# Kernel optimization log

Hardware: AMD Instinct MI355X
Metric: run time of the kernel (lower is better)

Reference implementation:

```python
import jax, jax.numpy as jnp
import numpy as np

NUM_GRAPHS = 1024
NODES_PER_GRAPH = 9
EDGES_PER_GRAPH = NODES_PER_GRAPH * (NODES_PER_GRAPH - 1)  # 72, fully connected no self-loops
N = NUM_GRAPHS * NODES_PER_GRAPH
E = NUM_GRAPHS * EDGES_PER_GRAPH
POS_DIM = 64
HID = 256          # gnn_hidden_dim / common_gnn_dim
S1_FEAT = HID      # stage1 feature_dim (after projection)
S1_INT = S1_FEAT + POS_DIM           # 320
S2_FEAT = 2 * HID                    # 512 (two scales concatenated)
S2_OUT = 2 * HID                     # 512
S2_INT = S2_FEAT + POS_DIM           # 576
LN_EPS = 1e-5
SM_EPS = 1e-16  # PyG softmax eps


def _dense(x, w, b):
    return x @ w + b


def _layer_norm(x, g, b):
    mu = jnp.mean(x, axis=-1, keepdims=True)
    var = jnp.mean(jnp.square(x - mu), axis=-1, keepdims=True)
    return (x - mu) * jax.lax.rsqrt(var + LN_EPS) * g + b


def _segment_softmax(logits, idx, n):
    # logits: [E,1]; normalize over edges sharing the same destination node
    m = jax.ops.segment_max(logits, idx, num_segments=n)
    e = jnp.exp(logits - m[idx])
    s = jax.ops.segment_sum(e, idx, num_segments=n)
    return e / (s[idx] + SM_EPS)


def _gnn_layer(x, pos, src, dst, n, p):
    # x: [N, F], pos: [N, P]; edges src->dst (PyG: edge_index[0]=src j, edge_index[1]=dst i)
    ix = jnp.concatenate([x, pos], axis=-1)            # integrated_x [N, F+P]
    ii, ij = ix[dst], ix[src]                          # integrated_x_i / _j per edge
    # pairwise_fn(integrated_x_j, integrated_x_i) -> mlp(cat([integrated_x_i, integrated_x_j]))
    pw_in = jnp.concatenate([ii, ij], axis=-1)         # [E, 2*(F+P)]
    rel = _dense(jax.nn.gelu(_dense(pw_in, p['pw1_w'], p['pw1_b']), approximate=False),
                 p['pw2_w'], p['pw2_b'])               # [E, out]
    att_in = jnp.concatenate([x[dst], x[src], pos[dst], pos[src]], axis=-1)
    logits = _dense(jax.nn.leaky_relu(_dense(att_in, p['att1_w'], p['att1_b']), 0.01),
                    p['att2_w'], p['att2_b'])          # [E, 1]
    attw = _segment_softmax(logits, dst, n)
    aggr = jax.ops.segment_sum(attw * rel, dst, num_segments=n)  # [N, out]
    upd = jax.nn.gelu(_dense(jnp.concatenate([ix, aggr], axis=-1), p['upd_w'], p['upd_b']),
                      approximate=False)
    h = _dense(ix, p['skip_w'], p['skip_b']) + upd
    return _layer_norm(h, p['ln_g'], p['ln_b'])


def _glorot(key, shape):
    fan_in, fan_out = shape[0], shape[1]
    lim = np.sqrt(6.0 / (fan_in + fan_out))
    return jax.random.uniform(key, shape, jnp.float32, -lim, lim)


def setup_inputs() -> dict:
    key = jax.random.key(0)
    ks = iter(jax.random.split(key, 64))

    feat_low = jax.random.normal(next(ks), (N, 512), jnp.float32)
    feat_high = jax.random.normal(next(ks), (N, 1024), jnp.float32)
    batch_indices = jnp.repeat(jnp.arange(NUM_GRAPHS), NODES_PER_GRAPH).astype(jnp.int32)

    # fully connected (no self loop) edges within each 9-node graph
    loc = np.array([(j, i) for i in range(NODES_PER_GRAPH) for j in range(NODES_PER_GRAPH) if i != j],
                   dtype=np.int64)  # (src, dst)
    off = np.repeat(np.arange(NUM_GRAPHS) * NODES_PER_GRAPH, EDGES_PER_GRAPH)
    src = np.tile(loc[:, 0], NUM_GRAPHS) + off
    dst = np.tile(loc[:, 1], NUM_GRAPHS) + off
    edge_index = jnp.asarray(np.stack([src, dst]), dtype=jnp.int32)  # [2, E]

    inp = dict(feat_low=feat_low, feat_high=feat_high,
               batch_indices=batch_indices, edge_index=edge_index)

    inp['pos_table'] = jax.random.normal(next(ks), (NODES_PER_GRAPH, POS_DIM), jnp.float32)
    inp['proj_low_w'] = _glorot(next(ks), (512, HID)); inp['proj_low_b'] = jnp.zeros((HID,), jnp.float32)
    inp['proj_high_w'] = _glorot(next(ks), (1024, HID)); inp['proj_high_b'] = jnp.zeros((HID,), jnp.float32)

    def layer_params(pref, fdim, pdim, out):
        integ = fdim + pdim
        d = {}
        d[pref + 'pw1_w'] = _glorot(next(ks), (2 * integ, out)); d[pref + 'pw1_b'] = jnp.zeros((out,), jnp.float32)
        d[pref + 'pw2_w'] = _glorot(next(ks), (out, out)); d[pref + 'pw2_b'] = jnp.zeros((out,), jnp.float32)
        d[pref + 'att1_w'] = _glorot(next(ks), (2 * fdim + 2 * pdim, out)); d[pref + 'att1_b'] = jnp.zeros((out,), jnp.float32)
        d[pref + 'att2_w'] = _glorot(next(ks), (out, 1)); d[pref + 'att2_b'] = jnp.zeros((1,), jnp.float32)
        d[pref + 'upd_w'] = _glorot(next(ks), (integ + out, out)); d[pref + 'upd_b'] = jnp.zeros((out,), jnp.float32)
        d[pref + 'ln_g'] = jnp.ones((out,), jnp.float32); d[pref + 'ln_b'] = jnp.zeros((out,), jnp.float32)
        d[pref + 'skip_w'] = _glorot(next(ks), (integ, out)); d[pref + 'skip_b'] = jnp.zeros((out,), jnp.float32)
        return d

    inp.update(layer_params('s1_', S1_FEAT, POS_DIM, HID))
    inp.update(layer_params('s2_', S2_FEAT, POS_DIM, S2_OUT))

    inp['cls1_w'] = _glorot(next(ks), (S2_OUT, HID)); inp['cls1_b'] = jnp.zeros((HID,), jnp.float32)
    inp['cls2_w'] = _glorot(next(ks), (HID, 1)); inp['cls2_b'] = jnp.zeros((1,), jnp.float32)
    return inp


def _forward(feat_low, feat_high, pos_table,
             proj_low_w, proj_low_b, proj_high_w, proj_high_b,
             s1, s2, cls1_w, cls1_b, cls2_w, cls2_b,
             batch_indices, edge_index):
    src, dst = edge_index[0], edge_index[1]
    pos_ids = jnp.tile(jnp.arange(NODES_PER_GRAPH), NUM_GRAPHS)
    pos = pos_table[pos_ids]                                  # [N, P]
    h_low = _gnn_layer(_dense(feat_low, proj_low_w, proj_low_b), pos, src, dst, N, s1)
    h_high = _gnn_layer(_dense(feat_high, proj_high_w, proj_high_b), pos, src, dst, N, s1)
    unified = jnp.concatenate([h_low, h_high], axis=-1)       # [N, 512]
    h2 = _gnn_layer(unified, pos, src, dst, N, s2)            # [N, 512]
    pooled = jax.ops.segment_sum(h2, batch_indices, num_segments=NUM_GRAPHS)
    hid = jax.nn.gelu(_dense(pooled, cls1_w, cls1_b), approximate=False)
    return _dense(hid, cls2_w, cls2_b)                        # [G, 1]


S1_KEYS = ['pw1_w', 'pw1_b', 'pw2_w', 'pw2_b', 'att1_w', 'att1_b', 'att2_w', 'att2_b',
           'upd_w', 'upd_b', 'ln_g', 'ln_b', 'skip_w', 'skip_b']


def reference(feat_low, feat_high, batch_indices, edge_index, pos_table,
              proj_low_w, proj_low_b, proj_high_w, proj_high_b,
              s1_pw1_w, s1_pw1_b, s1_pw2_w, s1_pw2_b, s1_att1_w, s1_att1_b,
              s1_att2_w, s1_att2_b, s1_upd_w, s1_upd_b, s1_ln_g, s1_ln_b,
              s1_skip_w, s1_skip_b,
              s2_pw1_w, s2_pw1_b, s2_pw2_w, s2_pw2_b, s2_att1_w, s2_att1_b,
              s2_att2_w, s2_att2_b, s2_upd_w, s2_upd_b, s2_ln_g, s2_ln_b,
              s2_skip_w, s2_skip_b,
              cls1_w, cls1_b, cls2_w, cls2_b):
    s1 = dict(zip(S1_KEYS, [s1_pw1_w, s1_pw1_b, s1_pw2_w, s1_pw2_b, s1_att1_w, s1_att1_b,
                            s1_att2_w, s1_att2_b, s1_upd_w, s1_upd_b, s1_ln_g, s1_ln_b,
                            s1_skip_w, s1_skip_b]))
    s2 = dict(zip(S1_KEYS, [s2_pw1_w, s2_pw1_b, s2_pw2_w, s2_pw2_b, s2_att1_w, s2_att1_b,
                            s2_att2_w, s2_att2_b, s2_upd_w, s2_upd_b, s2_ln_g, s2_ln_b,
                            s2_skip_w, s2_skip_b]))
    return _forward(feat_low, feat_high, pos_table,
                    proj_low_w, proj_low_b, proj_high_w, proj_high_b,
                    s1, s2, cls1_w, cls1_b, cls2_w, cls2_b,
                    batch_indices, edge_index)
```

## Files before the change

### kernel.cpp

```cpp
#include <hip/hip_runtime.h>
#include <math.h>

#define NUM_GRAPHS 1024
#define NPG 9
#define NN 9216
#define NN2 18432
#define POSD 64

typedef __attribute__((ext_vector_type(8))) short bf16x8;
typedef __attribute__((ext_vector_type(4))) float f32x4;

__device__ __forceinline__ float gelu_f(float x) {
    return 0.5f * x * (1.0f + erff(x * 0.70710678118654752f));
}
__device__ __forceinline__ float gelu_fast(float x) {
    float y = 0.7978845608f * x * (1.0f + 0.044715f * x * x);
    float t = __expf(-2.0f * fabsf(y));
    float r = (1.0f - t) / (1.0f + t);
    r = copysignf(r, y);
    return 0.5f * x * (1.0f + r);
}
__device__ __forceinline__ ushort f2b(float v) {
    unsigned u = __float_as_uint(v);
    return (ushort)((u + 0x7fffu + ((u >> 16) & 1u)) >> 16);
}
__device__ __forceinline__ float b2f(ushort u) {
    return __uint_as_float(((unsigned)u) << 16);
}
__device__ __forceinline__ void gload16(const ushort* g, ushort* l) {
    __builtin_amdgcn_global_load_lds((const __attribute__((address_space(1))) void*)g,
                                     (__attribute__((address_space(3))) void*)l, 16, 0, 0);
}

__global__ __launch_bounds__(256, 3) void mgemm(
    const ushort* __restrict__ A, int lda,
    const ushort* __restrict__ Wt, int ldw,
    const float* __restrict__ bias1,
    const float* __restrict__ prow, int ldp,
    float* outF, ushort* outB, int ldo,
    long partStride, int K)
{
    __shared__ ushort sA[3][128 * 32];
    __shared__ ushort sB[3][128 * 32];
    const int wv = threadIdx.x >> 6, lane = threadIdx.x & 63;
    const int rh = wv & 1, ch = wv >> 1;

    const int GX = gridDim.x;
    const int nwg = GX * gridDim.y;
    const int flat = blockIdx.y * GX + blockIdx.x;
    const int swq = nwg >> 3, swr = nwg & 7;
    const int xcd = flat & 7, posi = flat >> 3;
    const int tix = (xcd < swr ? xcd * (swq + 1) : swr * (swq + 1) + (xcd - swr) * swq) + posi;
    const int m0 = (tix / GX) * 128, n0 = (tix % GX) * 128;

    const int koff = blockIdx.z * K;

    f32x4 acc[4][4];
#pragma unroll
    for (int i = 0; i < 4; i++)
#pragma unroll
        for (int j = 0; j < 4; j++) acc[i][j] = (f32x4){0.f, 0.f, 0.f, 0.f};

    const ushort* Ab = A + (size_t)m0 * lda + koff;
    const ushort* Wb = Wt + (size_t)n0 * ldw + koff;
    if (outF) outF += (size_t)blockIdx.z * partStride;

    auto stage = [&](int b, int k0) {
#pragma unroll
        for (int i = 0; i < 2; i++) {
            int c = wv * 2 + i;
            int u = c * 64 + lane;
            int row = u >> 2, p = u & 3;
            int q = (p - (row >> 1)) & 3;
            gload16(Ab + (size_t)row * lda + k0 + q * 8, sA[b] + c * 512);
            gload16(Wb + (size_t)row * ldw + k0 + q * 8, sB[b] + c * 512);
        }
    };

    const int nsteps = K >> 5;
    stage(0, 0);
    stage(1, 32);
    int cur = 0;
    for (int s = 0; s < nsteps; s++) {
        if (s + 1 < nsteps) {
            asm volatile("s_waitcnt vmcnt(4)" ::: "memory");
        } else {
            asm volatile("s_waitcnt vmcnt(0)" ::: "memory");
        }
        __builtin_amdgcn_s_barrier();
        __builtin_amdgcn_sched_barrier(0);
        if (s + 2 < nsteps) {
            int nb = cur + 2; if (nb >= 3) nb -= 3;
            stage(nb, (s + 2) << 5);
        }

        const int qg = lane >> 4;
        bf16x8 af[4], bfr[4];
#pragma unroll
        for (int bi = 0; bi < 4; bi++) {
            int r = rh * 64 + bi * 16 + (lane & 15);
            af[bi] = *(const bf16x8*)(sA[cur] + (r * 4 + ((qg + (r >> 1)) & 3)) * 8);
        }
#pragma unroll
        for (int bj = 0; bj < 4; bj++) {
            int r = ch * 64 + bj * 16 + (lane & 15);
            bfr[bj] = *(const bf16x8*)(sB[cur] + (r * 4 + ((qg + (r >> 1)) & 3)) * 8);
        }
        __builtin_amdgcn_s_setprio(1);
#pragma unroll
        for (int bi = 0; bi < 4; bi++)
#pragma unroll
            for (int bj = 0; bj < 4; bj++)
                acc[bi][bj] = __builtin_amdgcn_mfma_f32_16x16x32_bf16(
                    af[bi], bfr[bj], acc[bi][bj], 0, 0, 0);
        __builtin_amdgcn_s_setprio(0);
        __builtin_amdgcn_sched_barrier(0);
        cur++; if (cur >= 3) cur -= 3;
    }

    float* sP = (float*)sA;
    const bool haveP = (prow != 0);
    if (haveP) {
        __syncthreads();
        for (int i = threadIdx.x; i < 9 * 128; i += 256) {
            int rr = i >> 7, c = i & 127;
            sP[rr * 129 + c] = prow[(size_t)rr * ldp + n0 + c] + bias1[n0 + c];
        }
        __syncthreads();
    }

#pragma unroll
    for (int bi = 0; bi < 4; bi++) {
#pragma unroll
        for (int r = 0; r < 4; r++) {
            int m = m0 + rh * 64 + bi * 16 + (lane >> 4) * 4 + r;
            int r9 = m % 9;
#pragma unroll
            for (int bj = 0; bj < 4; bj++) {
                int nc = ch * 64 + bj * 16 + (lane & 15);
                int n = n0 + nc;
                float v = acc[bi][bj][r];
                if (haveP) v += sP[r9 * 129 + nc];
                if (outF) outF[(size_t)m * ldo + n] = v;
                if (outB) outB[(size_t)m * ldo + n] = f2b(v);
            }
        }
    }
}

#define NJOBS 16
struct TJobsArg {
    const float* src[NJOBS];
    long dst[NJOBS];
    int K[NJOBS], N[NJOBS], off0[NJOBS], ldo[NJOBS];
};

__global__ __launch_bounds__(256) void tw_kernel(TJobsArg ja, ushort* wbuf)
{
    int j = blockIdx.y;
    int K = ja.K[j], N = ja.N[j];
    int tk = K >> 5, tn = N >> 5;
    int t = blockIdx.x;
    if (t >= tk * tn) return;
    int kt = t % tk, nt = t / tk;
    const float* src = ja.src[j];
    ushort* out = wbuf + ja.dst[j];
    int ldo = ja.ldo[j];
    __shared__ float L[32][33];
    int r = threadIdx.x >> 5, c = threadIdx.x & 31;
#pragma unroll
    for (int rr = 0; rr < 4; rr++) {
        int k = kt * 32 + rr * 8 + r;
        L[rr * 8 + r][c] = src[(size_t)(ja.off0[j] + k) * N + nt * 32 + c];
    }
    __syncthreads();
#pragma unroll
    for (int rr = 0; rr < 4; rr++) {
        int n = nt * 32 + rr * 8 + r;
        out[(size_t)n * ldo + kt * 32 + c] = f2b(L[c][rr * 8 + r]);
    }
}

__global__ void pjred_kernel(const float* __restrict__ PT,
                             const float* __restrict__ bl, const float* __restrict__ bh,
                             ushort* __restrict__ ixa1)
{
    int i = blockIdx.x * 256 + threadIdx.x;
    if (i >= NN2 * 64) return;
    int n = i >> 6, cq = i & 63;
    const float *p0, *p1, *bb; int r;
    if (n < NN) { p0 = PT; p1 = PT + (size_t)NN * 256; bb = bl; r = n; }
    else { p0 = PT + (size_t)2 * NN * 256; p1 = PT + (size_t)3 * NN * 256; bb = bh; r = n - NN; }
    float4 a = ((const float4*)(p0 + (size_t)r * 256))[cq];
    float4 b = ((const float4*)(p1 + (size_t)r * 256))[cq];
    float4 bs = ((const float4*)bb)[cq];
    ushort4 o;
    o.x = f2b(a.x + b.x + bs.x); o.y = f2b(a.y + b.y + bs.y);
    o.z = f2b(a.z + b.z + bs.z); o.w = f2b(a.w + b.w + bs.w);
    ((ushort4*)(ixa1 + (size_t)n * 512))[cq] = o;
}

__global__ __launch_bounds__(256) void edge_kernel(
    const ushort* __restrict__ PB, const float* __restrict__ att2_w,
    ushort* __restrict__ Gout, int ldG, float* __restrict__ S, int O, int cshift)
{
    __shared__ ushort sPB[9 * 2048];
    __shared__ float sAw[512];
    __shared__ float logits[72];
    __shared__ float aw[72];
    const int g = blockIdx.x;
    const int tid = threadIdx.x, lane = tid & 63, wave = tid >> 6;
    const int O4 = O * 4, O5 = O * 5;
    const int cpr = O >> 7;
    const int total = 9 * cpr;
    const ushort* gbase = PB + (size_t)g * 9 * O5;

    for (int i = wave; i < total; i += 4) {
        int row = i / cpr, co = i - row * cpr;
        gload16(gbase + (size_t)row * O5 + co * 512 + lane * 8, sPB + i * 512);
    }
    for (int c = tid; c < O; c += 256) sAw[c] = att2_w[c];
    __syncthreads();

    for (int e = wave; e < 72; e += 4) {
        int d = e >> 3, k = e & 7;
        int s = k + (k >= d);
        const ushort* ad = sPB + d * O4 + 2 * O;
        const ushort* as = sPB + s * O4 + 3 * O;
        float p = 0.f;
        for (int c0 = lane * 4; c0 < O; c0 += 256) {
            ushort4 a4 = *(const ushort4*)(ad + c0);
            ushort4 s4 = *(const ushort4*)(as + c0);
            const ushort* ap = (const ushort*)&a4;
            const ushort* sp = (const ushort*)&s4;
#pragma unroll
            for (int j = 0; j < 4; j++) {
                float v = b2f(ap[j]) + b2f(sp[j]);
                v = v > 0.f ? v : 0.01f * v;
                p += v * sAw[c0 + j];
            }
        }
#pragma unroll
        for (int off = 32; off; off >>= 1) p += __shfl_down(p, off, 64);
        if (lane == 0) logits[e] = p;
    }
    __syncthreads();

    if (tid < 9) {
        float m = -INFINITY;
#pragma unroll
        for (int k = 0; k < 8; k++) m = fmaxf(m, logits[tid * 8 + k]);
        float s = 0.f, ee[8];
#pragma unroll
        for (int k = 0; k < 8; k++) { ee[k] = expf(logits[tid * 8 + k] - m); s += ee[k]; }
        float inv = 1.0f / (s + 1e-16f);
#pragma unroll
        for (int k = 0; k < 8; k++) aw[tid * 8 + k] = ee[k] * inv;
        S[g * 9 + tid] = s * inv;
    }
    __syncthreads();

    const int nch = O >> 3;
    for (int idx = tid; idx < 9 * nch; idx += 256) {
        int n = idx >> cshift, cc = idx & (nch - 1);
        bf16x8 pdv = *(const bf16x8*)(sPB + n * O4 + cc * 8);
        const ushort* pp = (const ushort*)&pdv;
        float acc8[8];
#pragma unroll
        for (int j = 0; j < 8; j++) acc8[j] = 0.f;
#pragma unroll
        for (int k = 0; k < 8; k++) {
            int s = k + (k >= n);
            float w = aw[n * 8 + k];
            bf16x8 psv = *(const bf16x8*)(sPB + s * O4 + O + cc * 8);
            const ushort* qp = (const ushort*)&psv;
#pragma unroll
            for (int j = 0; j < 8; j++)
                acc8[j] += w * gelu_fast(b2f(pp[j]) + b2f(qp[j]));
        }
        ushort o8[8];
#pragma unroll
        for (int j = 0; j < 8; j++) o8[j] = f2b(acc8[j]);
        *(bf16x8*)(Gout + (size_t)(g * 9 + n) * ldG + cc * 8) = *(const bf16x8*)o8;
    }
}

__global__ __launch_bounds__(256) void ln_kernel(
    const float* __restrict__ P0, const float* __restrict__ P1,
    const float* __restrict__ ub, const float* __restrict__ vb,
    const float* __restrict__ S, const float* __restrict__ posU,
    const ushort* __restrict__ PBs, int ld5,
    const float* __restrict__ gw, const float* __restrict__ bw,
    ushort* outB, int ldoB, int rowsplit, float* outF, int O)
{
    __shared__ float sm[4];
    const int n = blockIdx.x, tid = threadIdx.x;
    const int lane = tid & 63, wid = tid >> 6;
    const float* p0 = P0 + (size_t)n * O;
    const float* p1 = P1 + (size_t)n * O;
    const ushort* sr = PBs + (size_t)n * ld5;
    const float* pu = posU + (size_t)(n % 9) * O;
    const float sv = S[n];
    const int cnt = O >> 8;

    float vals[2];
    float sum = 0.f;
#pragma unroll
    for (int i = 0; i < 2; i++) {
        if (i < cnt) {
            int c = tid + 256 * i;
            float t = p0[c] + p1[c] + ub[c] + vb[c] * sv + pu[c];
            vals[i] = gelu_f(t) + b2f(sr[c]);
            sum += vals[i];
        }
    }
#pragma unroll
    for (int off = 32; off; off >>= 1) sum += __shfl_down(sum, off, 64);
    if (lane == 0) sm[wid] = sum;
    __syncthreads();
    const float mu = (sm[0] + sm[1] + sm[2] + sm[3]) / (float)O;
    __syncthreads();

    float var = 0.f;
#pragma unroll
    for (int i = 0; i < 2; i++) {
        if (i < cnt) { float d = vals[i] - mu; var += d * d; }
    }
#pragma unroll
    for (int off = 32; off; off >>= 1) var += __shfl_down(var, off, 64);
    if (lane == 0) sm[wid] = var;
    __syncthreads();
    const float rstd = rsqrtf((sm[0] + sm[1] + sm[2] + sm[3]) / (float)O + 1e-5f);

    int orow = n, coloff = 0;
    if (n >= rowsplit) { orow = n - rowsplit; coloff = 256; }
#pragma unroll
    for (int i = 0; i < 2; i++) {
        if (i < cnt) {
            int c = tid + 256 * i;
            float v = (vals[i] - mu) * rstd * gw[c] + bw[c];
            if (outB) outB[(size_t)orow * ldoB + coloff + c] = f2b(v);
            if (outF) outF[(size_t)n * O + c] = v;
        }
    }
}

__global__ void prep_kernel(
    const float* __restrict__ pw1_b1, const float* __restrict__ att1_b1, const float* __restrict__ skip_b1,
    const float* __restrict__ pw1_b2, const float* __restrict__ att1_b2, const float* __restrict__ skip_b2,
    const float* __restrict__ pos_table,
    const float* __restrict__ s1_pw1, const float* __restrict__ s1_att, const float* __restrict__ s1_skp,
    const float* __restrict__ s2_pw1, const float* __restrict__ s2_att, const float* __restrict__ s2_skp,
    const float* __restrict__ pw2_b1, const float* __restrict__ upd_w1,
    const float* __restrict__ pw2_b2, const float* __restrict__ upd_w2,
    const float* __restrict__ pw2_w1, const float* __restrict__ pw2_w2,
    const float* __restrict__ feat_low, const float* __restrict__ feat_high,
    float* biasC1, float* biasC2,
    float* posPB1, float* posPB2, float* posU1, float* posU2,
    float* vb1, float* vb2, ushort* pw2f1, ushort* pw2f2, ushort* featB)
{
    int i = blockIdx.x * 256 + threadIdx.x;
    if (i < 1280) {
        float v;
        if (i < 256) v = pw1_b1[i];
        else if (i < 512) v = 0.f;
        else if (i < 768) v = att1_b1[i - 512];
        else if (i < 1024) v = 0.f;
        else v = skip_b1[i - 1024];
        biasC1[i] = v;
        return;
    }
    i -= 1280;
    if (i < 2560) {
        float v;
        if (i < 512) v = pw1_b2[i];
        else if (i < 1024) v = 0.f;
        else if (i < 1536) v = att1_b2[i - 1024];
        else if (i < 2048) v = 0.f;
        else v = skip_b2[i - 2048];
        biasC2[i] = v;
        return;
    }
    i -= 2560;
    if (i < 9 * 1280) {
        int r = i / 1280, n = i - r * 1280;
        int sec = n >> 8, c = n & 255;
        const float* src; int row0;
        if (sec == 0) { src = s1_pw1; row0 = 256; }
        else if (sec == 1) { src = s1_pw1; row0 = 576; }
        else if (sec == 2) { src = s1_att; row0 = 512; }
        else if (sec == 3) { src = s1_att; row0 = 576; }
        else { src = s1_skp; row0 = 256; }
        float a = 0.f;
        for (int k = 0; k < 64; k++) a += pos_table[r * 64 + k] * src[(size_t)(row0 + k) * 256 + c];
        posPB1[i] = a;
        return;
    }
    i -= 9 * 1280;
    if (i < 9 * 2560) {
        int r = i / 2560, n = i - r * 2560;
        int sec = n >> 9, c = n & 511;
        const float* src; int row0;
        if (sec == 0) { src = s2_pw1; row0 = 512; }
        else if (sec == 1) { src = s2_pw1; row0 = 1088; }
        else if (sec == 2) { src = s2_att; row0 = 1024; }
        else if (sec == 3) { src = s2_att; row0 = 1088; }
        else { src = s2_skp; row0 = 512; }
        float a = 0.f;
        for (int k = 0; k < 64; k++) a += pos_table[r * 64 + k] * src[(size_t)(row0 + k) * 512 + c];
        posPB2[i] = a;
        return;
    }
    i -= 9 * 2560;
    if (i < 9 * 256) {
        int r = i >> 8, c = i & 255;
        float a = 0.f;
        for (int k = 0; k < 64; k++) a += pos_table[r * 64 + k] * upd_w1[(size_t)(256 + k) * 256 + c];
        posU1[i] = a;
        return;
    }
    i -= 9 * 256;
    if (i < 9 * 512) {
        int r = i >> 9, c = i & 511;
        float a = 0.f;
        for (int k = 0; k < 64; k++) a += pos_table[r * 64 + k] * upd_w2[(size_t)(512 + k) * 512 + c];
        posU2[i] = a;
        return;
    }
    i -= 9 * 512;
    if (i < 256) {
        float a = 0.f;
        for (int j = 0; j < 256; j++) a += pw2_b1[j] * upd_w1[(size_t)(320 + j) * 256 + i];
        vb1[i] = a;
        return;
    }
    i -= 256;
    if (i < 512) {
        float a = 0.f;
        for (int j = 0; j < 512; j++) a += pw2_b2[j] * upd_w2[(size_t)(576 + j) * 512 + i];
        vb2[i] = a;
        return;
    }
    i -= 512;
    if (i < 256 * 256) { pw2f1[i] = f2b(pw2_w1[i]); return; }
    i -= 256 * 256;
    if (i < 512 * 512) { pw2f2[i] = f2b(pw2_w2[i]); return; }
    i -= 512 * 512;
    if (i < NN * 512 / 4) {
        float4 v = ((const float4*)feat_low)[i];
        ushort4 o;
        o.x = f2b(v.x); o.y = f2b(v.y); o.z = f2b(v.z); o.w = f2b(v.w);
        ((ushort4*)featB)[i] = o;
        return;
    }
    i -= NN * 512 / 4;
    if (i < NN * 1024 / 4) {
        float4 v = ((const float4*)feat_high)[i];
        ushort4 o;
        o.x = f2b(v.x); o.y = f2b(v.y); o.z = f2b(v.z); o.w = f2b(v.w);
        ((ushort4*)(featB + (size_t)NN * 512))[i] = o;
    }
}

__global__ __launch_bounds__(256) void head_kernel(
    const float* __restrict__ h2,
    const float* __restrict__ cls1_w, const float* __restrict__ cls1_b,
    const float* __restrict__ cls2_w, const float* __restrict__ cls2_b,
    float* __restrict__ out)
{
    __shared__ float pooled[4][512];
    __shared__ float hid[4][256];
    const int b = blockIdx.x, tid = threadIdx.x;

    for (int idx = tid; idx < 4 * 512; idx += 256) {
        int gi = idx >> 9, c = idx & 511;
        const float* base = h2 + (size_t)((b * 4 + gi) * 9) * 512 + c;
        float s = 0.f;
#pragma unroll
        for (int k = 0; k < NPG; k++) s += base[(size_t)k * 512];
        pooled[gi][c] = s;
    }
    __syncthreads();

    {
        float acc[4] = {0.f, 0.f, 0.f, 0.f};
        for (int c = 0; c < 512; c++) {
            float w = cls1_w[(size_t)c * 256 + tid];
#pragma unroll
            for (int gi = 0; gi < 4; gi++) acc[gi] += pooled[gi][c] * w;
        }
        float bb = cls1_b[tid];
#pragma unroll
        for (int gi = 0; gi < 4; gi++) hid[gi][tid] = gelu_f(acc[gi] + bb);
    }
    __syncthreads();

    {
        int gi = tid >> 6, lane = tid & 63;
        float p = 0.f;
#pragma unroll
        for (int i = 0; i < 4; i++) p += hid[gi][lane + 64 * i] * cls2_w[lane + 64 * i];
#pragma unroll
        for (int off = 32; off; off >>= 1) p += __shfl_down(p, off, 64);
        if (lane == 0) out[b * 4 + gi] = p + cls2_b[0];
    }
}

static inline void mg(hipStream_t st, int M, int N, int K,
                      const ushort* A, int lda, const ushort* Wt, int ldw,
                      const float* bias1, const float* prow, int ldp,
                      float* outF, ushort* outB, int ldo,
                      int nz, long partStride)
{
    dim3 grid(N / 128, M / 128, nz);
    mgemm<<<grid, dim3(256), 0, st>>>(A, lda, Wt, ldw, bias1, prow, ldp,
                                      outF, outB, ldo, partStride, K);
}

extern "C" void kernel_launch(void* const* d_in, const int* in_sizes, int n_in,
                              void* d_out, int out_size, void* d_ws, size_t ws_size,
                              hipStream_t stream)
{
    (void)in_sizes; (void)n_in; (void)out_size; (void)ws_size;
    const float* feat_low   = (const float*)d_in[0];
    const float* feat_high  = (const float*)d_in[1];
    const float* pos_table  = (const float*)d_in[4];
    const float* proj_low_w  = (const float*)d_in[5];
    const float* proj_low_b  = (const float*)d_in[6];
    const float* proj_high_w = (const float*)d_in[7];
    const float* proj_high_b = (const float*)d_in[8];
    const float* cls1_w = (const float*)d_in[37];
    const float* cls1_b = (const float*)d_in[38];
    const float* cls2_w = (const float*)d_in[39];
    const float* cls2_b = (const float*)d_in[40];
    float* out = (float*)d_out;

    const float* s1_pw1 = (const float*)d_in[9];
    const float* s1_att = (const float*)d_in[13];
    const float* s1_upd = (const float*)d_in[17];
    const float* s1_skp = (const float*)d_in[21];
    const float* s2_pw1 = (const float*)d_in[23];
    const float* s2_att = (const float*)d_in[27];
    const float* s2_upd = (const float*)d_in[31];
    const float* s2_skp = (const float*)d_in[35];

    const float* att2_w1 = (const float*)d_in[15];
    const float* upd_b1  = (const float*)d_in[18];
    const float* ln_g1   = (const float*)d_in[19];
    const float* ln_b1   = (const float*)d_in[20];
    const float* att2_w2 = (const float*)d_in[29];
    const float* upd_b2  = (const float*)d_in[32];
    const float* ln_g2   = (const float*)d_in[33];
    const float* ln_b2   = (const float*)d_in[34];

    char* base = (char*)d_ws;
    size_t cur = 0;
    auto alloc = [&](size_t bytes) { void* p = base + cur; cur += (bytes + 255) & ~(size_t)255; return p; };
    void*   PBreg = alloc((size_t)NN * 2560 * 2);
    ushort* PB    = (ushort*)PBreg;
    ushort* featB = (ushort*)PBreg;
    void*   IX1reg = alloc((size_t)NN2 * 512 * 2);
    ushort* ixa1  = (ushort*)IX1reg;
    float*  h2    = (float*)IX1reg;
    ushort* ixa2  = (ushort*)alloc((size_t)NN * 1024 * 2);
    float*  PT    = (float*)alloc((size_t)4 * NN * 256 * 4);
    float*  S     = (float*)alloc((size_t)NN2 * 4);
    float*  biasC1 = (float*)alloc(1280 * 4);
    float*  biasC2 = (float*)alloc(2560 * 4);
    float*  posPB1 = (float*)alloc(9 * 1280 * 4);
    float*  posPB2 = (float*)alloc(9 * 2560 * 4);
    float*  posU1  = (float*)alloc(9 * 256 * 4);
    float*  posU2  = (float*)alloc(9 * 512 * 4);
    float*  vb1   = (float*)alloc(256 * 4);
    float*  vb2   = (float*)alloc(512 * 4);
    ushort* wbuf  = (ushort*)alloc((size_t)3400000 * 2);

    TJobsArg ja;
    long woff[16];
    {
        struct J { const float* s; int K, N, off0, ldo; long sz; };
        J js[NJOBS] = {
            {proj_low_w,  512, 256, 0, 512, 512L * 256},
            {proj_high_w, 1024, 256, 0, 1024, 1024L * 256},
            {s1_pw1, 256, 256, 0, 256, 256L * 256},
            {s1_pw1, 256, 256, 320, 256, 256L * 256},
            {s1_att, 256, 256, 0, 256, 256L * 256},
            {s1_att, 256, 256, 256, 256, 256L * 256},
            {s1_skp, 256, 256, 0, 256, 256L * 256},
            {s1_upd, 256, 256, 0, 512, 512L * 256},
            {s1_upd, 256, 256, 320, 256, 256L * 256},
            {s2_pw1, 512, 512, 0, 512, 512L * 512},
            {s2_pw1, 512, 512, 576, 512, 512L * 512},
            {s2_att, 512, 512, 0, 512, 512L * 512},
            {s2_att, 512, 512, 512, 512, 512L * 512},
            {s2_skp, 512, 512, 0, 512, 512L * 512},
            {s2_upd, 512, 512, 0, 1024, 1024L * 512},
            {s2_upd, 512, 512, 576, 512, 512L * 512},
        };
        long off = 0;
        for (int i = 0; i < NJOBS; i++) {
            ja.src[i] = js[i].s; ja.K[i] = js[i].K; ja.N[i] = js[i].N;
            ja.off0[i] = js[i].off0; ja.ldo[i] = js[i].ldo;
            ja.dst[i] = off; woff[i] = off;
            off += js[i].sz;
        }
    }
    long pw2off1 = woff[15] + 512L * 512;
    long pw2off2 = pw2off1 + 256L * 256;
    tw_kernel<<<dim3(256, NJOBS), dim3(256), 0, stream>>>(ja, wbuf);

    ushort* wBig5_1 = wbuf + woff[2];
    ushort* updW1   = wbuf + woff[7];
    ushort* updbT1  = wbuf + woff[8];
    ushort* wBig5_2 = wbuf + woff[9];
    ushort* updW2   = wbuf + woff[14];
    ushort* updbT2  = wbuf + woff[15];
    ushort* pw2f1   = wbuf + pw2off1;
    ushort* pw2f2   = wbuf + pw2off2;

    {
        long tot = 1280 + 2560 + 9 * 1280 + 9 * 2560 + 9 * 256 + 9 * 512
                 + 256 + 512 + 256 * 256 + 512 * 512
                 + (long)NN * 512 / 4 + (long)NN * 1024 / 4;
        prep_kernel<<<dim3((unsigned)((tot + 255) / 256)), dim3(256), 0, stream>>>(
            (const float*)d_in[10], (const float*)d_in[14], (const float*)d_in[22],
            (const float*)d_in[24], (const float*)d_in[28], (const float*)d_in[36],
            pos_table,
            s1_pw1, s1_att, s1_skp, s2_pw1, s2_att, s2_skp,
            (const float*)d_in[12], s1_upd, (const float*)d_in[26], s2_upd,
            (const float*)d_in[11], (const float*)d_in[25],
            feat_low, feat_high,
            biasC1, biasC2, posPB1, posPB2, posU1, posU2, vb1, vb2, pw2f1, pw2f2, featB);
    }

    mg(stream, 256, 256, 256, updbT1, 256, pw2f1, 256, 0, 0, 0, 0, updW1 + 256, 512, 1, 0);
    mg(stream, 512, 512, 512, updbT2, 512, pw2f2, 512, 0, 0, 0, 0, updW2 + 512, 1024, 1, 0);

    mg(stream, NN, 256, 256, featB, 512, wbuf + woff[0], 512, 0, 0, 0,
       PT, 0, 256, 2, (long)NN * 256);
    mg(stream, NN, 256, 512, featB + (size_t)NN * 512, 1024, wbuf + woff[1], 1024, 0, 0, 0,
       PT + (size_t)2 * NN * 256, 0, 256, 2, (long)NN * 256);
    pjred_kernel<<<dim3(NN2 * 64 / 256), dim3(256), 0, stream>>>(PT, proj_low_b, proj_high_b, ixa1);

    mg(stream, NN2, 1280, 256, ixa1, 512, wBig5_1, 256, biasC1, posPB1, 1280, 0, PB, 1280, 1, 0);
    edge_kernel<<<dim3(2 * NUM_GRAPHS), dim3(256), 0, stream>>>(
        PB, att2_w1, ixa1 + 256, 512, S, 256, 5);
    mg(stream, NN2, 256, 256, ixa1, 512, updW1, 512, 0, 0, 0, PT, 0, 256, 2, (long)NN2 * 256);
    ln_kernel<<<dim3(NN2), dim3(256), 0, stream>>>(
        PT, PT + (size_t)NN2 * 256, upd_b1, vb1, S, posU1,
        PB + 4 * 256, 1280, ln_g1, ln_b1, ixa2, 1024, NN, 0, 256);

    mg(stream, NN, 2560, 512, ixa2, 1024, wBig5_2, 512, biasC2, posPB2, 2560, 0, PB, 2560, 1, 0);
    edge_kernel<<<dim3(NUM_GRAPHS), dim3(256), 0, stream>>>(
        PB, att2_w2, ixa2 + 512, 1024, S, 512, 6);
    mg(stream, NN, 512, 512, ixa2, 1024, updW2, 1024, 0, 0, 0, PT, 0, 512, 2, (long)NN * 512);
    ln_kernel<<<dim3(NN), dim3(256), 0, stream>>>(
        PT, PT + (size_t)NN * 512, upd_b2, vb2, S, posU2,
        PB + 4 * 512, 2560, ln_g2, ln_b2, 0, 0, 1 << 30, h2, 512);

    head_kernel<<<dim3(NUM_GRAPHS / 4), dim3(256), 0, stream>>>(h2, cls1_w, cls1_b, cls2_w, cls2_b, out);
}
```

Before: 552.2 us.

## Fuse projection GEMMs with bias/bf16 epilogue and drop split-K for update GEMMs

Replaces the two split-K projection GEMMs and the separate reduction kernel with one batched pjgemm kernel. It uses a triple-buffered LDS pipeline with swizzled loads and XCD-aware tile remapping, and writes bias-added bf16 directly into the stage-1 input buffer. The update GEMMs now run with a full K and a single split, so ln_kernel reads one partial buffer instead of summing two. This removes the fp32 partial-sum round trips and a kernel launch, but the update GEMMs have fewer workgroups and so less parallelism.

```diff
diff --git a/kernel.cpp b/kernel.cpp
--- a/kernel.cpp
+++ b/kernel.cpp
@@ -143,6 +143,118 @@
                 if (haveP) v += sP[r9 * 129 + nc];
                 if (outF) outF[(size_t)m * ldo + n] = v;
                 if (outB) outB[(size_t)m * ldo + n] = f2b(v);
+            }
+        }
+    }
+}
+
+struct PJArg {
+    const ushort* A[2];
+    const ushort* W[2];
+    const float*  bias[2];
+    ushort*       out[2];
+    int lda[2], K[2];
+};
+
+__global__ __launch_bounds__(256, 3) void pjgemm(PJArg pa)
+{
+    __shared__ ushort sA[3][128 * 32];
+    __shared__ ushort sB[3][128 * 32];
+    const int z = blockIdx.z;
+    const ushort* __restrict__ A  = pa.A[z];
+    const ushort* __restrict__ Wt = pa.W[z];
+    const float*  __restrict__ bias = pa.bias[z];
+    ushort* out = pa.out[z];
+    const int lda = pa.lda[z], ldw = lda, K = pa.K[z];
+
+    const int wv = threadIdx.x >> 6, lane = threadIdx.x & 63;
+    const int rh = wv & 1, ch = wv >> 1;
+
+    const int GX = gridDim.x;
+    const int nwg = GX * gridDim.y;
+    const int flat = blockIdx.y * GX + blockIdx.x;
+    const int swq = nwg >> 3, swr = nwg & 7;
+    const int xcd = flat & 7, posi = flat >> 3;
+    const int tix = (xcd < swr ? xcd * (swq + 1) : swr * (swq + 1) + (xcd - swr) * swq) + posi;
+    const int m0 = (tix / GX) * 128, n0 = (tix % GX) * 128;
+
+    f32x4 acc[4][4];
+#pragma unroll
+    for (int i = 0; i < 4; i++)
+#pragma unroll
+        for (int j = 0; j < 4; j++) acc[i][j] = (f32x4){0.f, 0.f, 0.f, 0.f};
+
+    const ushort* Ab = A + (size_t)m0 * lda;
+    const ushort* Wb = Wt + (size_t)n0 * ldw;
+
+    auto stage = [&](int b, int k0) {
+#pragma unroll
+        for (int i = 0; i < 2; i++) {
+            int c = wv * 2 + i;
+            int u = c * 64 + lane;
+            int row = u >> 2, p = u & 3;
+            int q = (p - (row >> 1)) & 3;
+            gload16(Ab + (size_t)row * lda + k0 + q * 8, sA[b] + c * 512);
+            gload16(Wb + (size_t)row * ldw + k0 + q * 8, sB[b] + c * 512);
+        }
+    };
+
+    const int nsteps = K >> 5;
+    stage(0, 0);
+    stage(1, 32);
+    int cur = 0;
+    for (int s = 0; s < nsteps; s++) {
+        if (s + 1 < nsteps) {
+            asm volatile("s_waitcnt vmcnt(4)" ::: "memory");
+        } else {
+            asm volatile("s_waitcnt vmcnt(0)" ::: "memory");
+        }
+        __builtin_amdgcn_s_barrier();
+        __builtin_amdgcn_sched_barrier(0);
+        if (s + 2 < nsteps) {
+            int nb = cur + 2; if (nb >= 3) nb -= 3;
+            stage(nb, (s + 2) << 5);
+        }
+
+        const int qg = lane >> 4;
+        bf16x8 af[4], bfr[4];
+#pragma unroll
+        for (int bi = 0; bi < 4; bi++) {
+            int r = rh * 64 + bi * 16 + (lane & 15);
+            af[bi] = *(const bf16x8*)(sA[cur] + (r * 4 + ((qg + (r >> 1)) & 3)) * 8);
+        }
+#pragma unroll
+        for (int bj = 0; bj < 4; bj++) {
+            int r = ch * 64 + bj * 16 + (lane & 15);
+            bfr[bj] = *(const bf16x8*)(sB[cur] + (r * 4 + ((qg + (r >> 1)) & 3)) * 8);
+        }
+        __builtin_amdgcn_s_setprio(1);
+#pragma unroll
+        for (int bi = 0; bi < 4; bi++)
+#pragma unroll
+            for (int bj = 0; bj < 4; bj++)
+                acc[bi][bj] = __builtin_amdgcn_mfma_f32_16x16x32_bf16(
+                    af[bi], bfr[bj], acc[bi][bj], 0, 0, 0);
+        __builtin_amdgcn_s_setprio(0);
+        __builtin_amdgcn_sched_barrier(0);
+        cur++; if (cur >= 3) cur -= 3;
+    }
+
+    float* sBias = (float*)sA;
+    __syncthreads();
+    if (threadIdx.x < 128) sBias[threadIdx.x] = bias[n0 + threadIdx.x];
+    __syncthreads();
+
+#pragma unroll
+    for (int bi = 0; bi < 4; bi++) {
+#pragma unroll
+        for (int r = 0; r < 4; r++) {
+            int m = m0 + rh * 64 + bi * 16 + (lane >> 4) * 4 + r;
+#pragma unroll
+            for (int bj = 0; bj < 4; bj++) {
+                int nc = ch * 64 + bj * 16 + (lane & 15);
+                float v = acc[bi][bj][r] + sBias[nc];
+                out[(size_t)m * 512 + n0 + nc] = f2b(v);
             }
         }
     }
@@ -181,25 +293,6 @@
     }
 }
 
-__global__ void pjred_kernel(const float* __restrict__ PT,
-                             const float* __restrict__ bl, const float* __restrict__ bh,
-                             ushort* __restrict__ ixa1)
-{
-    int i = blockIdx.x * 256 + threadIdx.x;
-    if (i >= NN2 * 64) return;
-    int n = i >> 6, cq = i & 63;
-    const float *p0, *p1, *bb; int r;
-    if (n < NN) { p0 = PT; p1 = PT + (size_t)NN * 256; bb = bl; r = n; }
-    else { p0 = PT + (size_t)2 * NN * 256; p1 = PT + (size_t)3 * NN * 256; bb = bh; r = n - NN; }
-    float4 a = ((const float4*)(p0 + (size_t)r * 256))[cq];
-    float4 b = ((const float4*)(p1 + (size_t)r * 256))[cq];
-    float4 bs = ((const float4*)bb)[cq];
-    ushort4 o;
-    o.x = f2b(a.x + b.x + bs.x); o.y = f2b(a.y + b.y + bs.y);
-    o.z = f2b(a.z + b.z + bs.z); o.w = f2b(a.w + b.w + bs.w);
-    ((ushort4*)(ixa1 + (size_t)n * 512))[cq] = o;
-}
-
 __global__ __launch_bounds__(256) void edge_kernel(
     const ushort* __restrict__ PB, const float* __restrict__ att2_w,
     ushort* __restrict__ Gout, int ldG, float* __restrict__ S, int O, int cshift)
@@ -297,7 +390,7 @@
     const int n = blockIdx.x, tid = threadIdx.x;
     const int lane = tid & 63, wid = tid >> 6;
     const float* p0 = P0 + (size_t)n * O;
-    const float* p1 = P1 + (size_t)n * O;
+    const float* p1 = P1 ? P1 + (size_t)n * O : 0;
     const ushort* sr = PBs + (size_t)n * ld5;
     const float* pu = posU + (size_t)(n % 9) * O;
     const float sv = S[n];
@@ -309,7 +402,7 @@
     for (int i = 0; i < 2; i++) {
         if (i < cnt) {
             int c = tid + 256 * i;
-            float t = p0[c] + p1[c] + ub[c] + vb[c] * sv + pu[c];
+            float t = p0[c] + (p1 ? p1[c] : 0.f) + ub[c] + vb[c] * sv + pu[c];
             vals[i] = gelu_f(t) + b2f(sr[c]);
             sum += vals[i];
         }
@@ -636,26 +729,33 @@
     mg(stream, 256, 256, 256, updbT1, 256, pw2f1, 256, 0, 0, 0, 0, updW1 + 256, 512, 1, 0);
     mg(stream, 512, 512, 512, updbT2, 512, pw2f2, 512, 0, 0, 0, 0, updW2 + 512, 1024, 1, 0);
 
-    mg(stream, NN, 256, 256, featB, 512, wbuf + woff[0], 512, 0, 0, 0,
-       PT, 0, 256, 2, (long)NN * 256);
-    mg(stream, NN, 256, 512, featB + (size_t)NN * 512, 1024, wbuf + woff[1], 1024, 0, 0, 0,
-       PT + (size_t)2 * NN * 256, 0, 256, 2, (long)NN * 256);
-    pjred_kernel<<<dim3(NN2 * 64 / 256), dim3(256), 0, stream>>>(PT, proj_low_b, proj_high_b, ixa1);
+    {
+        PJArg pa;
+        pa.A[0] = featB;                      pa.lda[0] = 512;  pa.K[0] = 512;
+        pa.A[1] = featB + (size_t)NN * 512;   pa.lda[1] = 1024; pa.K[1] = 1024;
+        pa.W[0] = wbuf + woff[0];
+        pa.W[1] = wbuf + woff[1];
+        pa.bias[0] = proj_low_b;
+        pa.bias[1] = proj_high_b;
+        pa.out[0] = ixa1;
+        pa.out[1] = ixa1 + (size_t)NN * 512;
+        pjgemm<<<dim3(2, NN / 128, 2), dim3(256), 0, stream>>>(pa);
+    }
 
     mg(stream, NN2, 1280, 256, ixa1, 512, wBig5_1, 256, biasC1, posPB1, 1280, 0, PB, 1280, 1, 0);
     edge_kernel<<<dim3(2 * NUM_GRAPHS), dim3(256), 0, stream>>>(
         PB, att2_w1, ixa1 + 256, 512, S, 256, 5);
-    mg(stream, NN2, 256, 256, ixa1, 512, updW1, 512, 0, 0, 0, PT, 0, 256, 2, (long)NN2 * 256);
+    mg(stream, NN2, 256, 512, ixa1, 512, updW1, 512, 0, 0, 0, PT, 0, 256, 1, 0);
     ln_kernel<<<dim3(NN2), dim3(256), 0, stream>>>(
-        PT, PT + (size_t)NN2 * 256, upd_b1, vb1, S, posU1,
+        PT, 0, upd_b1, vb1, S, posU1,
         PB + 4 * 256, 1280, ln_g1, ln_b1, ixa2, 1024, NN, 0, 256);
 
     mg(stream, NN, 2560, 512, ixa2, 1024, wBig5_2, 512, biasC2, posPB2, 2560, 0, PB, 2560, 1, 0);
     edge_kernel<<<dim3(NUM_GRAPHS), dim3(256), 0, stream>>>(
         PB, att2_w2, ixa2 + 512, 1024, S, 512, 6);
-    mg(stream, NN, 512, 512, ixa2, 1024, updW2, 1024, 0, 0, 0, PT, 0, 512, 2, (long)NN * 512);
+    mg(stream, NN, 512, 1024, ixa2, 1024, updW2, 1024, 0, 0, 0, PT, 0, 512, 1, 0);
     ln_kernel<<<dim3(NN), dim3(256), 0, stream>>>(
-        PT, PT + (size_t)NN * 512, upd_b2, vb2, S, posU2,
+        PT, 0, upd_b2, vb2, S, posU2,
         PB + 4 * 512, 2560, ln_g2, ln_b2, 0, 0, 1 << 30, h2, 512);
 
     head_kernel<<<dim3(NUM_GRAPHS / 4), dim3(256), 0, stream>>>(h2, cls1_w, cls1_b, cls2_w, cls2_b, out);
```

Result: no change. 561.8 us (+1.7%).
